# Kernel optimization log

Measured on AMD Instinct MI355X. Metric: run time of the kernel, lower is better.

The kernel has to match this reference:

```python
import jax, jax.numpy as jnp
import numpy as np

B, N, H, HID, P = 4, 1024, 16, 64, 2


def setup_inputs() -> dict:
    key = jax.random.key(0)
    ks = jax.random.split(key, 8)
    positions = jax.random.normal(ks[0], (B, N, P), dtype=jnp.float32)
    key_padding_mask = jax.random.bernoulli(ks[1], 0.1, (B, N))
    # MLP params (Linear stores weight as (out,in) in torch; we keep (in,out) and matmul)
    s1 = 1.0 / np.sqrt(P)
    s2 = 1.0 / np.sqrt(HID)
    W1 = jax.random.uniform(ks[2], (P, HID), jnp.float32, -s1, s1)
    b1 = jax.random.uniform(ks[3], (HID,), jnp.float32, -s1, s1)
    W2 = jax.random.uniform(ks[4], (HID, HID), jnp.float32, -s2, s2)
    b2 = jax.random.uniform(ks[5], (HID,), jnp.float32, -s2, s2)
    W3 = jax.random.uniform(ks[6], (HID, H), jnp.float32, -s2, s2)
    b3 = jax.random.uniform(ks[7], (H,), jnp.float32, -s2, s2)
    return {"positions": positions, "key_padding_mask": key_padding_mask,
            "W1": W1, "b1": b1, "W2": W2, "b2": b2, "W3": W3, "b3": b3}


def reference(positions, key_padding_mask, W1, b1, W2, b2, W3, b3):
    # rel_pos[b, i, j] = pos[b, j] - pos[b, i]  -> (B, N, N, 2)
    rel = positions[:, None, :, :] - positions[:, :, None, :]
    h = jax.nn.relu(rel @ W1 + b1)          # (B, N, N, HID)
    h = jax.nn.relu(h @ W2 + b2)            # (B, N, N, HID)
    bias = h @ W3 + b3                      # (B, N, N, H)
    bias = jnp.transpose(bias, (0, 3, 1, 2))  # (B, H, N, N)
    # zero out rows/cols touching padded tokens
    combined = key_padding_mask[:, None, None, :] | key_padding_mask[:, None, :, None]
    bias = jnp.where(combined, 0.0, bias)
    return bias
```

## Files before the change

kernel.cpp:

```cpp
#include <hip/hip_runtime.h>
#include <hip/hip_bf16.h>
#include <hip/hip_fp16.h>

#define B_   4
#define N_   1024
#define H_   16
#define HID_ 64
#define TI   16
#define JH   512

typedef float    f32x4  __attribute__((ext_vector_type(4)));
typedef __fp16   fp16x2 __attribute__((ext_vector_type(2)));
typedef _Float16 f16x8  __attribute__((ext_vector_type(8)));
typedef unsigned int u32;

union F16x8U { u32 u[4]; f16x8 v; };

static __device__ __forceinline__ u32 pk(float a, float b) {
    union { fp16x2 f; u32 u; } r;
    r.f = __builtin_amdgcn_cvt_pkrtz(a, b);
    return r.u;
}
static __device__ __forceinline__ u32 pkadd_relu(u32 a, u32 b) {
    union { u32 u; fp16x2 f; } x, y, r;
    x.u = a; y.u = b;
    fp16x2 z = { (__fp16)0.f, (__fp16)0.f };
    fp16x2 s = x.f + y.f;
    r.f = __builtin_elementwise_max(s, z);
    return r.u;
}
static __device__ __forceinline__ u32 pkcvt_relu(float a, float b) {
    union { fp16x2 f; u32 u; } r;
    fp16x2 z = { (__fp16)0.f, (__fp16)0.f };
    fp16x2 s = __builtin_amdgcn_cvt_pkrtz(a, b);
    r.f = __builtin_elementwise_max(s, z);
    return r.u;
}

__global__ __launch_bounds__(512, 2) void RelativePositionalBias_kernel(
    const float* __restrict__ pos,
    const int*   __restrict__ mask,
    const float* __restrict__ W1,
    const float* __restrict__ b1,
    const float* __restrict__ W2,
    const float* __restrict__ b2,
    const float* __restrict__ W3,
    const float* __restrict__ b3,
    float* __restrict__ out)
{
    __shared__ __align__(16) u32 ujL[JH][32];
    __shared__ __align__(16) u32 uinL[TI][32];

    const int b   = blockIdx.z;
    const int i0  = blockIdx.y * TI;
    const int j0  = blockIdx.x * JH;
    const int tid = threadIdx.x;
    const int w = tid >> 6;
    const int l = tid & 63;
    const int g = l >> 4;
    const int c = l & 15;

    for (int it = tid; it < (JH + TI) * 8; it += 512) {
        int r  = it >> 3;
        int qq = it & 7;
        int k0 = qq * 8;
        int tok = (r < JH) ? (j0 + r) : (i0 + (r - JH));
        float2 p  = *(const float2*)&pos[(b * N_ + tok) * 2];
        float4 a0 = *(const float4*)&W1[k0];
        float4 a1 = *(const float4*)&W1[k0 + 4];
        float4 c0 = *(const float4*)&W1[HID_ + k0];
        float4 c1 = *(const float4*)&W1[HID_ + k0 + 4];
        float u0 = p.x*a0.x + p.y*c0.x, u1 = p.x*a0.y + p.y*c0.y;
        float u2 = p.x*a0.z + p.y*c0.z, u3 = p.x*a0.w + p.y*c0.w;
        float u4 = p.x*a1.x + p.y*c1.x, u5 = p.x*a1.y + p.y*c1.y;
        float u6 = p.x*a1.z + p.y*c1.z, u7 = p.x*a1.w + p.y*c1.w;
        const int col = ((qq ^ (r & 7)) << 2);
        uint4 o;
        if (r < JH) {
            o.x = pk(u0, u1); o.y = pk(u2, u3); o.z = pk(u4, u5); o.w = pk(u6, u7);
            *(uint4*)&ujL[r][col] = o;
        } else {
            float4 ba = *(const float4*)&b1[k0];
            float4 bb = *(const float4*)&b1[k0 + 4];
            o.x = pk(ba.x - u0, ba.y - u1); o.y = pk(ba.z - u2, ba.w - u3);
            o.z = pk(bb.x - u4, bb.y - u5); o.w = pk(bb.z - u6, bb.w - u7);
            *(uint4*)&uinL[r - JH][col] = o;
        }
    }

    F16x8U W2f[2][4];
    #pragma unroll
    for (int s = 0; s < 2; ++s)
        #pragma unroll
        for (int n = 0; n < 4; ++n)
            #pragma unroll
            for (int e = 0; e < 8; ++e)
                W2f[s][n].v[e] = (_Float16)W2[(32*s + 8*g + e) * HID_ + 16*n + c];

    F16x8U W3g[2];
    #pragma unroll
    for (int s = 0; s < 2; ++s)
        #pragma unroll
        for (int e = 0; e < 8; ++e)
            W3g[s].v[e] = (_Float16)W3[(32*s + 16*(e>>2) + 4*g + (e&3)) * H_ + c];

    f32x4 b2v[4];
    #pragma unroll
    for (int n = 0; n < 4; ++n)
        b2v[n] = *(const f32x4*)&b2[16*n + 4*g];
    const float b3v = b3[c];

    const int* maskb = &mask[b * N_ + i0];
    u32 mrow = 0;
    #pragma unroll
    for (int tt = 0; tt < 4; ++tt) {
        int4 m = *(const int4*)&maskb[tt * 4];
        mrow |= (m.x ? 1u : 0u) << (4*tt);
        mrow |= (m.y ? 1u : 0u) << (4*tt + 1);
        mrow |= (m.z ? 1u : 0u) << (4*tt + 2);
        mrow |= (m.w ? 1u : 0u) << (4*tt + 3);
    }

    f32x4 mmul[4];
    #pragma unroll
    for (int jj = 0; jj < 4; ++jj) {
        int4 mj = *(const int4*)&mask[b * N_ + j0 + 64*w + 16*jj + 4*g];
        mmul[jj][0] = mj.x ? 0.f : 1.f;
        mmul[jj][1] = mj.y ? 0.f : 1.f;
        mmul[jj][2] = mj.z ? 0.f : 1.f;
        mmul[jj][3] = mj.w ? 0.f : 1.f;
    }

    float* const planeBase = out + ((size_t)(b*H_ + c) << 20) + ((size_t)i0 << 10)
                                 + (size_t)(j0 + 64*w + 4*g);

    __syncthreads();

    const f32x4 zero4 = { 0.f, 0.f, 0.f, 0.f };

    for (int t = 0; t < TI; ++t) {
        float* const rowp = planeBase + ((size_t)t << 10);

        if ((mrow >> t) & 1) {
            #pragma unroll
            for (int jj = 0; jj < 4; ++jj)
                *(f32x4*)(rowp + 16*jj) = zero4;
            continue;
        }

        const int tb = t & 7;
        const uint4 uiA = *(const uint4*)&uinL[t][(g ^ tb) << 2];
        const uint4 uiB = *(const uint4*)&uinL[t][((4 + g) ^ tb) << 2];

        #pragma unroll
        for (int jj = 0; jj < 4; ++jj) {
            const int jrow = 64*w + 16*jj + c;
            const int jb = c & 7;
            const uint4 pjA = *(const uint4*)&ujL[jrow][(g ^ jb) << 2];
            const uint4 pjB = *(const uint4*)&ujL[jrow][((4 + g) ^ jb) << 2];

            F16x8U A1[2];
            A1[0].u[0] = pkadd_relu(pjA.x, uiA.x);
            A1[0].u[1] = pkadd_relu(pjA.y, uiA.y);
            A1[0].u[2] = pkadd_relu(pjA.z, uiA.z);
            A1[0].u[3] = pkadd_relu(pjA.w, uiA.w);
            A1[1].u[0] = pkadd_relu(pjB.x, uiB.x);
            A1[1].u[1] = pkadd_relu(pjB.y, uiB.y);
            A1[1].u[2] = pkadd_relu(pjB.z, uiB.z);
            A1[1].u[3] = pkadd_relu(pjB.w, uiB.w);

            f32x4 acc[4];
            #pragma unroll
            for (int n = 0; n < 4; ++n) {
                acc[n] = __builtin_amdgcn_mfma_f32_16x16x32_f16(W2f[0][n].v, A1[0].v, b2v[n], 0, 0, 0);
                acc[n] = __builtin_amdgcn_mfma_f32_16x16x32_f16(W2f[1][n].v, A1[1].v, acc[n], 0, 0, 0);
            }

            F16x8U A3[2];
            #pragma unroll
            for (int s = 0; s < 2; ++s) {
                A3[s].u[0] = pkcvt_relu(acc[2*s][0],     acc[2*s][1]);
                A3[s].u[1] = pkcvt_relu(acc[2*s][2],     acc[2*s][3]);
                A3[s].u[2] = pkcvt_relu(acc[2*s + 1][0], acc[2*s + 1][1]);
                A3[s].u[3] = pkcvt_relu(acc[2*s + 1][2], acc[2*s + 1][3]);
            }

            f32x4 acc3 = { b3v, b3v, b3v, b3v };
            acc3 = __builtin_amdgcn_mfma_f32_16x16x32_f16(A3[0].v, W3g[0].v, acc3, 0, 0, 0);
            acc3 = __builtin_amdgcn_mfma_f32_16x16x32_f16(A3[1].v, W3g[1].v, acc3, 0, 0, 0);

            *(f32x4*)(rowp + 16*jj) = acc3 * mmul[jj];
        }
    }
}

extern "C" void kernel_launch(void* const* d_in, const int* in_sizes, int n_in,
                              void* d_out, int out_size, void* d_ws, size_t ws_size,
                              hipStream_t stream) {
    const float* pos  = (const float*)d_in[0];
    const int*   mask = (const int*)d_in[1];
    const float* W1   = (const float*)d_in[2];
    const float* b1   = (const float*)d_in[3];
    const float* W2   = (const float*)d_in[4];
    const float* b2   = (const float*)d_in[5];
    const float* W3   = (const float*)d_in[6];
    const float* b3   = (const float*)d_in[7];
    float* out = (float*)d_out;

    dim3 grid(N_ / JH, N_ / TI, B_);
    RelativePositionalBias_kernel<<<grid, dim3(512), 0, stream>>>(
        pos, mask, W1, b1, W2, b2, W3, b3, out);
}
```

Before: 57.42 us.

## Stage output tiles through LDS for contiguous row stores and shrink blocks

```diff
diff --git a/kernel.cpp b/kernel.cpp
--- a/kernel.cpp
+++ b/kernel.cpp
@@ -7,7 +7,8 @@
 #define H_   16
 #define HID_ 64
 #define TI   16
-#define JH   512
+#define JH   256
+#define PST  72
 
 typedef float    f32x4  __attribute__((ext_vector_type(4)));
 typedef __fp16   fp16x2 __attribute__((ext_vector_type(2)));
@@ -37,7 +38,7 @@
     return r.u;
 }
 
-__global__ __launch_bounds__(512, 2) void RelativePositionalBias_kernel(
+__global__ __launch_bounds__(256, 3) void RelativePositionalBias_kernel(
     const float* __restrict__ pos,
     const int*   __restrict__ mask,
     const float* __restrict__ W1,
@@ -48,8 +49,10 @@
     const float* __restrict__ b3,
     float* __restrict__ out)
 {
-    __shared__ __align__(16) u32 ujL[JH][32];
+    __shared__ __align__(16) u32 shm[JH * 32];
     __shared__ __align__(16) u32 uinL[TI][32];
+    u32 (*ujL)[32] = (u32(*)[32])shm;
+    float* const bounce = (float*)shm;
 
     const int b   = blockIdx.z;
     const int i0  = blockIdx.y * TI;
@@ -60,7 +63,7 @@
     const int g = l >> 4;
     const int c = l & 15;
 
-    for (int it = tid; it < (JH + TI) * 8; it += 512) {
+    for (int it = tid; it < (JH + TI) * 8; it += 256) {
         int r  = it >> 3;
         int qq = it & 7;
         int k0 = qq * 8;
@@ -131,20 +134,36 @@
         mmul[jj][3] = mj.w ? 0.f : 1.f;
     }
 
-    float* const planeBase = out + ((size_t)(b*H_ + c) << 20) + ((size_t)i0 << 10)
-                                 + (size_t)(j0 + 64*w + 4*g);
+    float* const stBase = out + ((size_t)(b*H_ + (l >> 4)) << 20)
+                              + ((size_t)i0 << 10)
+                              + (size_t)(j0 + 64*w + 4*(l & 15));
+
+    float* const wslice  = bounce + w * (16 * PST);
+    float* const depBase = wslice + c * PST + 4*g;
+    const float* const gathBase = wslice + (l >> 4) * PST + 4*(l & 15);
 
     __syncthreads();
 
+    uint4 pjA[4], pjB[4];
+    const int jb = c & 7;
+    #pragma unroll
+    for (int jj = 0; jj < 4; ++jj) {
+        const int jrow = 64*w + 16*jj + c;
+        pjA[jj] = *(const uint4*)&ujL[jrow][(g ^ jb) << 2];
+        pjB[jj] = *(const uint4*)&ujL[jrow][((4 + g) ^ jb) << 2];
+    }
+
+    __syncthreads();
+
     const f32x4 zero4 = { 0.f, 0.f, 0.f, 0.f };
 
     for (int t = 0; t < TI; ++t) {
-        float* const rowp = planeBase + ((size_t)t << 10);
+        float* const rowp = stBase + ((size_t)t << 10);
 
         if ((mrow >> t) & 1) {
             #pragma unroll
-            for (int jj = 0; jj < 4; ++jj)
-                *(f32x4*)(rowp + 16*jj) = zero4;
+            for (int s = 0; s < 4; ++s)
+                *(f32x4*)(rowp + ((size_t)s << 22)) = zero4;
             continue;
         }
 
@@ -154,20 +173,15 @@
 
         #pragma unroll
         for (int jj = 0; jj < 4; ++jj) {
-            const int jrow = 64*w + 16*jj + c;
-            const int jb = c & 7;
-            const uint4 pjA = *(const uint4*)&ujL[jrow][(g ^ jb) << 2];
-            const uint4 pjB = *(const uint4*)&ujL[jrow][((4 + g) ^ jb) << 2];
-
             F16x8U A1[2];
-            A1[0].u[0] = pkadd_relu(pjA.x, uiA.x);
-            A1[0].u[1] = pkadd_relu(pjA.y, uiA.y);
-            A1[0].u[2] = pkadd_relu(pjA.z, uiA.z);
-            A1[0].u[3] = pkadd_relu(pjA.w, uiA.w);
-            A1[1].u[0] = pkadd_relu(pjB.x, uiB.x);
-            A1[1].u[1] = pkadd_relu(pjB.y, uiB.y);
-            A1[1].u[2] = pkadd_relu(pjB.z, uiB.z);
-            A1[1].u[3] = pkadd_relu(pjB.w, uiB.w);
+            A1[0].u[0] = pkadd_relu(pjA[jj].x, uiA.x);
+            A1[0].u[1] = pkadd_relu(pjA[jj].y, uiA.y);
+            A1[0].u[2] = pkadd_relu(pjA[jj].z, uiA.z);
+            A1[0].u[3] = pkadd_relu(pjA[jj].w, uiA.w);
+            A1[1].u[0] = pkadd_relu(pjB[jj].x, uiB.x);
+            A1[1].u[1] = pkadd_relu(pjB[jj].y, uiB.y);
+            A1[1].u[2] = pkadd_relu(pjB[jj].z, uiB.z);
+            A1[1].u[3] = pkadd_relu(pjB[jj].w, uiB.w);
 
             f32x4 acc[4];
             #pragma unroll
@@ -189,7 +203,13 @@
             acc3 = __builtin_amdgcn_mfma_f32_16x16x32_f16(A3[0].v, W3g[0].v, acc3, 0, 0, 0);
             acc3 = __builtin_amdgcn_mfma_f32_16x16x32_f16(A3[1].v, W3g[1].v, acc3, 0, 0, 0);
 
-            *(f32x4*)(rowp + 16*jj) = acc3 * mmul[jj];
+            *(f32x4*)(depBase + 16*jj) = acc3 * mmul[jj];
+        }
+
+        #pragma unroll
+        for (int s = 0; s < 4; ++s) {
+            f32x4 v = *(const f32x4*)(gathBase + s * (4 * PST));
+            *(f32x4*)(rowp + ((size_t)s << 22)) = v;
         }
     }
 }
@@ -208,6 +228,6 @@
     float* out = (float*)d_out;
 
     dim3 grid(N_ / JH, N_ / TI, B_);
-    RelativePositionalBias_kernel<<<grid, dim3(512), 0, stream>>>(
+    RelativePositionalBias_kernel<<<grid, dim3(256), 0, stream>>>(
         pos, mask, W1, b1, W2, b2, W3, b3, out);
 }
```

Measured after the change: 57.56 us. Within noise of the previous version (+0.2%).
